# Optimization experiments

Measured on AMD Instinct MI355X. Metric: run time of the kernel, lower is better.

Reference implementation:

```python
import jax, jax.numpy as jnp
import numpy as np

B, T, IN, H, NB, OUT = 256, 2048, 128, 256, 4, 8
BS = H // NB  # branch size = 64


def setup_inputs() -> dict:
    key = jax.random.key(0)
    ks = jax.random.split(key, 7)
    x = jax.random.normal(ks[0], (B, T, IN), dtype=jnp.float32)
    Wb = jax.random.normal(ks[1], (NB, IN, BS), dtype=jnp.float32) * (1.0 / np.sqrt(IN))
    bb = jax.random.normal(ks[2], (NB, BS), dtype=jnp.float32) * 0.05
    Wo = jax.random.normal(ks[3], (H, OUT), dtype=jnp.float32) * (1.0 / np.sqrt(H))
    bo = jax.random.normal(ks[4], (OUT,), dtype=jnp.float32) * 0.05
    # tau_m ~ U(0,4); tau_n branch i ~ U(-4+2i, -1+2i) per the torch init
    tau_m = jax.random.uniform(ks[5], (H,), dtype=jnp.float32, minval=0.0, maxval=4.0)
    lo = (-4.0 + 2.0 * jnp.arange(NB, dtype=jnp.float32))[:, None]
    tau_n = lo + 3.0 * jax.random.uniform(ks[6], (NB, BS), dtype=jnp.float32)
    return {"x": x, "Wb": Wb, "bb": bb, "Wo": Wo, "bo": bo,
            "tau_m": tau_m, "tau_n": tau_n}


def reference(x, Wb, bb, Wo, bo, tau_m, tau_n):
    Bsz = x.shape[0]
    # Batch all per-step branch projections into one einsum: [B,T,NB,BS] -> [B,T,H]
    # (branch i writes slice [i*BS:(i+1)*BS], which matches the reshape order)
    D = jnp.einsum('bti,nis->btns', x, Wb) + bb  # [B,T,NB,BS]
    D = D.reshape(Bsz, x.shape[1], -1)           # [B,T,H]

    beta = jax.nn.sigmoid(tau_n).reshape(-1)     # [H], per-branch smoothing
    alpha = jax.nn.sigmoid(tau_m)                # [H]

    def step(carry, d_t):
        c, m = carry
        c = beta * c + (1.0 - beta) * d_t        # dendritic current EMA
        m = alpha * m + (1.0 - alpha) * c        # membrane EMA
        o = jax.nn.sigmoid(m @ Wo + bo)          # [B,OUT]
        return (c, m), o

    init = (jnp.zeros((Bsz, D.shape[-1]), D.dtype),
            jnp.zeros((Bsz, D.shape[-1]), D.dtype))
    _, outs = jax.lax.scan(step, init, jnp.swapaxes(D, 0, 1))  # outs: [T,B,OUT]
    return jnp.swapaxes(outs, 0, 1)              # [B,T,OUT]
```

## Files before the change

kernel.cpp:

```cpp
#include <hip/hip_runtime.h>
#include <hip/hip_bf16.h>
#include <math.h>

#define DEVFN __device__ __forceinline__

typedef __attribute__((ext_vector_type(8))) __bf16 bf16x8;
typedef __attribute__((ext_vector_type(8))) short s16x8;
typedef __attribute__((ext_vector_type(4))) float f32x4;
typedef __attribute__((ext_vector_type(4))) unsigned int u32x4;

constexpr int Tt    = 2048;
constexpr int INt   = 128;
constexpr int Ht    = 256;
constexpr int OUTt  = 8;
constexpr int TT    = 64;
constexpr int NTILE = 32;

union Frag {
  s16x8 s;
  bf16x8 b;
  u32x4 u;
};

DEVFN unsigned short f2bf(float f) {
  unsigned int u = __builtin_bit_cast(unsigned int, f);
  u += 0x7fffu + ((u >> 16) & 1u);
  return (unsigned short)(u >> 16);
}

DEVFN unsigned int pack2(float lo, float hi) {
  return (unsigned int)f2bf(lo) | ((unsigned int)f2bf(hi) << 16);
}

__global__
__attribute__((amdgpu_flat_work_group_size(1024, 1024)))
void sfnn_fused(
    const float* __restrict__ x, const float* __restrict__ Wb,
    const float* __restrict__ bb, const float* __restrict__ Wo,
    const float* __restrict__ bo, const float* __restrict__ tau_m,
    const float* __restrict__ tau_n, float* __restrict__ out)
{
  const int b    = blockIdx.x;
  const int tid  = threadIdx.x;
  const int lane = tid & 63;
  const int w    = tid >> 6;
  const int l16  = lane & 15;
  const int lhi  = lane >> 4;
  const int sid  = tid - 512;

  const int tg = w >> 3;
  const int hg = w & 7;

  __shared__ __align__(16) unsigned char  Xb[2][TT * 256];
  __shared__ __align__(16) float          DfT[Ht * TT];
  __shared__ __align__(16) unsigned short Mb[TT * Ht];
  __shared__ __align__(16) unsigned short WoT[16 * Ht];

  {
    const int j  = w;
    const int k0 = 4 * (tid & 63);
    float v0 = 0.f, v1 = 0.f, v2 = 0.f, v3 = 0.f;
    if (j < OUTt) {
      v0 = Wo[(k0 + 0) * OUTt + j]; v1 = Wo[(k0 + 1) * OUTt + j];
      v2 = Wo[(k0 + 2) * OUTt + j]; v3 = Wo[(k0 + 3) * OUTt + j];
    }
    unsigned long long pk = (unsigned long long)pack2(v0, v1) |
                            ((unsigned long long)pack2(v2, v3) << 32);
    *(unsigned long long*)(&WoT[j * 256 + (k0 ^ ((j & 7) << 3))]) = pk;
  }

  Frag Wf[2][4];
  #pragma unroll
  for (int nh = 0; nh < 2; ++nh) {
    const int h = 32 * hg + 16 * nh + l16;
    const int n = h >> 6, s = h & 63;
    #pragma unroll
    for (int ks = 0; ks < 4; ++ks) {
      #pragma unroll
      for (int j = 0; j < 8; ++j) {
        const int i = 32 * ks + 8 * lhi + j;
        Wf[nh][ks].s[j] = (short)f2bf(Wb[(n * 128 + i) * 64 + s]);
      }
    }
  }

  float beta = 0.f, alpha = 0.f, omb = 0.f, oma = 0.f, bbh = 0.f;
  if (tid < 256) {
    beta  = 1.f / (1.f + expf(-tau_n[tid]));
    alpha = 1.f / (1.f + expf(-tau_m[tid]));
    omb   = 1.f - beta;
    oma   = 1.f - alpha;
    bbh   = bb[tid];
  }
  float bo_l = 0.f;
  if (w >= 4 && w < 8) bo_l = (l16 < OUTt) ? bo[l16] : 0.f;

  const float* xb   = x   + (size_t)b * Tt * INt;
  float*       outb = out + (size_t)b * Tt * OUTt;

  float c_s = 0.f, m_s = 0.f;
  f32x4 dacc[2][2];
  f32x4 Q0, Q1;

  #define BAR() do {                                                       \
    asm volatile("s_waitcnt lgkmcnt(0)" ::: "memory");                     \
    __builtin_amdgcn_s_barrier();                                          \
  } while (0)

  #define WAITVM(N) do {                                                   \
    asm volatile("s_waitcnt vmcnt(" #N ")" ::: "memory");                  \
    __builtin_amdgcn_sched_barrier(0);                                     \
  } while (0)

  #define ISSUE(TILE) do {                                                 \
    const float* _p = xb + (size_t)(TILE) * (TT * INt) + 4 * (size_t)sid;  \
    asm volatile("global_load_dwordx4 %0, %1, off" : "=&v"(Q0) : "v"(_p));        \
    asm volatile("global_load_dwordx4 %0, %1, off" : "=&v"(Q1) : "v"(_p + 2048)); \
  } while (0)

  #define STAGE(BUF, TILE) do {                                            \
    const int kb = 8 * (sid & 31);                                         \
    WAITVM(0);                                                             \
    {                                                                      \
      const int t = (sid >> 5);                                            \
      unsigned long long pk = (unsigned long long)pack2(Q0.x, Q0.y) |      \
            ((unsigned long long)pack2(Q0.z, Q0.w) << 32);                 \
      *(unsigned long long*)(&Xb[BUF][t * 256 + (kb ^ ((t & 7) << 4))]) = pk; \
    }                                                                      \
    {                                                                      \
      const int t = 16 + (sid >> 5);                                       \
      unsigned long long pk = (unsigned long long)pack2(Q1.x, Q1.y) |      \
            ((unsigned long long)pack2(Q1.z, Q1.w) << 32);                 \
      *(unsigned long long*)(&Xb[BUF][t * 256 + (kb ^ ((t & 7) << 4))]) = pk; \
    }                                                                      \
    const float* _p2 = xb + (size_t)(TILE) * (TT * INt) + 4 * (size_t)sid; \
    asm volatile("global_load_dwordx4 %0, %1, off" : "=&v"(Q0) : "v"(_p2 + 4096)); \
    asm volatile("global_load_dwordx4 %0, %1, off" : "=&v"(Q1) : "v"(_p2 + 6144)); \
    WAITVM(0);                                                             \
    {                                                                      \
      const int t = 32 + (sid >> 5);                                       \
      unsigned long long pk = (unsigned long long)pack2(Q0.x, Q0.y) |      \
            ((unsigned long long)pack2(Q0.z, Q0.w) << 32);                 \
      *(unsigned long long*)(&Xb[BUF][t * 256 + (kb ^ ((t & 7) << 4))]) = pk; \
    }                                                                      \
    {                                                                      \
      const int t = 48 + (sid >> 5);                                       \
      unsigned long long pk = (unsigned long long)pack2(Q1.x, Q1.y) |      \
            ((unsigned long long)pack2(Q1.z, Q1.w) << 32);                 \
      *(unsigned long long*)(&Xb[BUF][t * 256 + (kb ^ ((t & 7) << 4))]) = pk; \
    }                                                                      \
  } while (0)

  #define GEMM(BUF) do {                                                   \
    _Pragma("unroll")                                                      \
    for (int tt = 0; tt < 2; ++tt) {                                       \
      _Pragma("unroll")                                                    \
      for (int nh = 0; nh < 2; ++nh) dacc[tt][nh] = f32x4{0.f,0.f,0.f,0.f};\
      const int row = 32 * tg + 16 * tt + l16;                             \
      const int rs = row * 256, sw = (row & 7) << 4;                       \
      _Pragma("unroll")                                                    \
      for (int ks = 0; ks < 4; ++ks) {                                     \
        Frag a;                                                            \
        a.u = *(const u32x4*)(&Xb[BUF][rs + ((64 * ks + 16 * lhi) ^ sw)]); \
        _Pragma("unroll")                                                  \
        for (int nh = 0; nh < 2; ++nh)                                     \
          dacc[tt][nh] = __builtin_amdgcn_mfma_f32_16x16x32_bf16(          \
              a.b, Wf[nh][ks].b, dacc[tt][nh], 0, 0, 0);                   \
      }                                                                    \
    }                                                                      \
  } while (0)

  #define WRITEDF() do {                                                   \
    _Pragma("unroll")                                                      \
    for (int tt = 0; tt < 2; ++tt)                                         \
      _Pragma("unroll")                                                    \
      for (int nh = 0; nh < 2; ++nh) {                                     \
        const int h = 32 * hg + 16 * nh + l16;                             \
        const int qi = 8 * tg + 4 * tt + lhi;                              \
        *(f32x4*)(&DfT[h * 64 + ((4 * qi) ^ ((h & 7) << 2))]) =            \
            dacc[tt][nh];                                                  \
      }                                                                    \
  } while (0)

  #define SCAN() do {                                                      \
    if (tid < 256) {                                                       \
      const int hb = tid * 64, dsw = (tid & 7) << 2;                       \
      _Pragma("unroll")                                                    \
      for (int gg = 0; gg < 4; ++gg) {                                     \
        f32x4 dv[4];                                                       \
        _Pragma("unroll")                                                  \
        for (int q = 0; q < 4; ++q)                                        \
          dv[q] = *(const f32x4*)(&DfT[hb + ((16 * gg + 4 * q) ^ dsw)]);   \
        _Pragma("unroll")                                                  \
        for (int q = 0; q < 4; ++q)                                        \
          _Pragma("unroll")                                                \
          for (int r = 0; r < 4; ++r) {                                    \
            const int t = 16 * gg + 4 * q + r;                             \
            const float d = dv[q][r] + bbh;                                \
            c_s = fmaf(beta, c_s, omb * d);                                \
            m_s = fmaf(alpha, m_s, oma * c_s);                             \
            Mb[t * 256 + (tid ^ ((t & 7) << 3))] = f2bf(m_s);              \
          }                                                                \
      }                                                                    \
    }                                                                      \
  } while (0)

  #define PROJ(TI) do {                                                    \
    const int tp = w - 4;                                                  \
    const int trow = 16 * tp + l16;                                        \
    const int mrb = trow * 256, msw = (trow & 7) << 3;                     \
    const int wrb = l16 * 256,  wsw = (l16 & 7) << 3;                      \
    f32x4 p = f32x4{0.f, 0.f, 0.f, 0.f};                                   \
    _Pragma("unroll")                                                      \
    for (int ks = 0; ks < 8; ++ks) {                                       \
      const int k0 = 32 * ks + 8 * lhi;                                    \
      Frag ma, wo;                                                         \
      ma.u = *(const u32x4*)(&Mb[mrb + (k0 ^ msw)]);                       \
      wo.u = *(const u32x4*)(&WoT[wrb + (k0 ^ wsw)]);                      \
      p = __builtin_amdgcn_mfma_f32_16x16x32_bf16(ma.b, wo.b, p, 0, 0, 0); \
    }                                                                      \
    if (l16 < OUTt) {                                                      \
      _Pragma("unroll")                                                    \
      for (int r = 0; r < 4; ++r) {                                        \
        const int t = 16 * tp + 4 * lhi + r;                               \
        outb[(size_t)((TI) * TT + t) * OUTt + l16] =                       \
            1.f / (1.f + __expf(-(p[r] + bo_l)));                          \
      }                                                                    \
    }                                                                      \
  } while (0)

  if (w >= 8) {
    ISSUE(0); STAGE(0, 0);
    ISSUE(1); STAGE(1, 1);
  }
  BAR();
  GEMM(0);

  #define ITER(I, DOPROJ, DOGEMM, DOIS) do {                               \
    if ((DOIS) && w >= 8) ISSUE((I) + 2);                                  \
    WRITEDF();                                                             \
    if ((DOPROJ) && w >= 4 && w < 8) PROJ((I) - 1);                        \
    if (DOGEMM) GEMM(((I) + 1) & 1);                                       \
    BAR();                                                         \
    SCAN();                                                                \
    if ((DOIS) && w >= 8) STAGE((I) & 1, (I) + 2);                         \
    BAR();                                                         \
  } while (0)

  ITER(0, 0, 1, 1);
  for (int I = 1; I <= 29; ++I) ITER(I, 1, 1, 1);
  ITER(30, 1, 1, 0);
  ITER(31, 1, 0, 0);
  if (w >= 4 && w < 8) PROJ(31);

  #undef ISSUE
  #undef STAGE
  #undef GEMM
  #undef WRITEDF
  #undef SCAN
  #undef PROJ
  #undef ITER
  #undef BAR
  #undef WAITVM
}

extern "C" void kernel_launch(void* const* d_in, const int* in_sizes, int n_in,
                              void* d_out, int out_size, void* d_ws, size_t ws_size,
                              hipStream_t stream) {
  const float* x     = (const float*)d_in[0];
  const float* Wb    = (const float*)d_in[1];
  const float* bb    = (const float*)d_in[2];
  const float* Wo    = (const float*)d_in[3];
  const float* bo    = (const float*)d_in[4];
  const float* tau_m = (const float*)d_in[5];
  const float* tau_n = (const float*)d_in[6];
  float* out = (float*)d_out;

  sfnn_fused<<<dim3(256), dim3(1024), 0, stream>>>(x, Wb, bb, Wo, bo, tau_m, tau_n, out);
}
```

Measured before the change: 102.0 us.

## Restructure into a three-stage software pipeline with smaller time tiles

```diff
diff --git a/kernel.cpp b/kernel.cpp
--- a/kernel.cpp
+++ b/kernel.cpp
@@ -13,8 +13,8 @@
 constexpr int INt   = 128;
 constexpr int Ht    = 256;
 constexpr int OUTt  = 8;
-constexpr int TT    = 64;
-constexpr int NTILE = 32;
+constexpr int TT    = 32;
+constexpr int NTILE = 64;
 
 union Frag {
   s16x8 s;
@@ -48,12 +48,9 @@
   const int lhi  = lane >> 4;
   const int sid  = tid - 512;
 
-  const int tg = w >> 3;
-  const int hg = w & 7;
-
-  __shared__ __align__(16) unsigned char  Xb[2][TT * 256];
-  __shared__ __align__(16) float          DfT[Ht * TT];
-  __shared__ __align__(16) unsigned short Mb[TT * Ht];
+  __shared__ __align__(16) unsigned char  Xb[3][TT * 256];
+  __shared__ __align__(16) float          DfT[2][Ht * TT];
+  __shared__ __align__(16) unsigned short Mb[2][TT * Ht];
   __shared__ __align__(16) unsigned short WoT[16 * Ht];
 
   {
@@ -69,17 +66,16 @@
     *(unsigned long long*)(&WoT[j * 256 + (k0 ^ ((j & 7) << 3))]) = pk;
   }
 
-  Frag Wf[2][4];
-  #pragma unroll
-  for (int nh = 0; nh < 2; ++nh) {
-    const int h = 32 * hg + 16 * nh + l16;
+  Frag Wf[4];
+  {
+    const int h = 16 * w + l16;
     const int n = h >> 6, s = h & 63;
     #pragma unroll
     for (int ks = 0; ks < 4; ++ks) {
       #pragma unroll
       for (int j = 0; j < 8; ++j) {
         const int i = 32 * ks + 8 * lhi + j;
-        Wf[nh][ks].s[j] = (short)f2bf(Wb[(n * 128 + i) * 64 + s]);
+        Wf[ks].s[j] = (short)f2bf(Wb[(n * 128 + i) * 64 + s]);
       }
     }
   }
@@ -93,14 +89,14 @@
     bbh   = bb[tid];
   }
   float bo_l = 0.f;
-  if (w >= 4 && w < 8) bo_l = (l16 < OUTt) ? bo[l16] : 0.f;
+  if (w == 4 || w == 5) bo_l = (l16 < OUTt) ? bo[l16] : 0.f;
 
   const float* xb   = x   + (size_t)b * Tt * INt;
   float*       outb = out + (size_t)b * Tt * OUTt;
 
   float c_s = 0.f, m_s = 0.f;
-  f32x4 dacc[2][2];
-  f32x4 Q0, Q1;
+  f32x4 dacc[2];
+  f32x4 QA0, QA1, QB0, QB1;
 
   #define BAR() do {                                                       \
     asm volatile("s_waitcnt lgkmcnt(0)" ::: "memory");                     \
@@ -112,15 +108,14 @@
     __builtin_amdgcn_sched_barrier(0);                                     \
   } while (0)
 
-  #define ISSUE(TILE) do {                                                 \
+  #define ISSUE(TILE, Q0, Q1) do {                                         \
     const float* _p = xb + (size_t)(TILE) * (TT * INt) + 4 * (size_t)sid;  \
     asm volatile("global_load_dwordx4 %0, %1, off" : "=&v"(Q0) : "v"(_p));        \
     asm volatile("global_load_dwordx4 %0, %1, off" : "=&v"(Q1) : "v"(_p + 2048)); \
   } while (0)
 
-  #define STAGE(BUF, TILE) do {                                            \
+  #define STAGEWR(BUF, Q0, Q1) do {                                        \
     const int kb = 8 * (sid & 31);                                         \
-    WAITVM(0);                                                             \
     {                                                                      \
       const int t = (sid >> 5);                                            \
       unsigned long long pk = (unsigned long long)pack2(Q0.x, Q0.y) |      \
@@ -133,79 +128,57 @@
             ((unsigned long long)pack2(Q1.z, Q1.w) << 32);                 \
       *(unsigned long long*)(&Xb[BUF][t * 256 + (kb ^ ((t & 7) << 4))]) = pk; \
     }                                                                      \
-    const float* _p2 = xb + (size_t)(TILE) * (TT * INt) + 4 * (size_t)sid; \
-    asm volatile("global_load_dwordx4 %0, %1, off" : "=&v"(Q0) : "v"(_p2 + 4096)); \
-    asm volatile("global_load_dwordx4 %0, %1, off" : "=&v"(Q1) : "v"(_p2 + 6144)); \
-    WAITVM(0);                                                             \
-    {                                                                      \
-      const int t = 32 + (sid >> 5);                                       \
-      unsigned long long pk = (unsigned long long)pack2(Q0.x, Q0.y) |      \
-            ((unsigned long long)pack2(Q0.z, Q0.w) << 32);                 \
-      *(unsigned long long*)(&Xb[BUF][t * 256 + (kb ^ ((t & 7) << 4))]) = pk; \
-    }                                                                      \
-    {                                                                      \
-      const int t = 48 + (sid >> 5);                                       \
-      unsigned long long pk = (unsigned long long)pack2(Q1.x, Q1.y) |      \
-            ((unsigned long long)pack2(Q1.z, Q1.w) << 32);                 \
-      *(unsigned long long*)(&Xb[BUF][t * 256 + (kb ^ ((t & 7) << 4))]) = pk; \
-    }                                                                      \
   } while (0)
 
   #define GEMM(BUF) do {                                                   \
     _Pragma("unroll")                                                      \
     for (int tt = 0; tt < 2; ++tt) {                                       \
-      _Pragma("unroll")                                                    \
-      for (int nh = 0; nh < 2; ++nh) dacc[tt][nh] = f32x4{0.f,0.f,0.f,0.f};\
-      const int row = 32 * tg + 16 * tt + l16;                             \
+      dacc[tt] = f32x4{0.f, 0.f, 0.f, 0.f};                                \
+      const int row = 16 * tt + l16;                                       \
       const int rs = row * 256, sw = (row & 7) << 4;                       \
       _Pragma("unroll")                                                    \
       for (int ks = 0; ks < 4; ++ks) {                                     \
         Frag a;                                                            \
         a.u = *(const u32x4*)(&Xb[BUF][rs + ((64 * ks + 16 * lhi) ^ sw)]); \
-        _Pragma("unroll")                                                  \
-        for (int nh = 0; nh < 2; ++nh)                                     \
-          dacc[tt][nh] = __builtin_amdgcn_mfma_f32_16x16x32_bf16(          \
-              a.b, Wf[nh][ks].b, dacc[tt][nh], 0, 0, 0);                   \
+        dacc[tt] = __builtin_amdgcn_mfma_f32_16x16x32_bf16(                \
+            a.b, Wf[ks].b, dacc[tt], 0, 0, 0);                             \
       }                                                                    \
     }                                                                      \
   } while (0)
 
-  #define WRITEDF() do {                                                   \
+  #define WRITEDF(BUF) do {                                                \
+    const int h = 16 * w + l16;                                            \
     _Pragma("unroll")                                                      \
-    for (int tt = 0; tt < 2; ++tt)                                         \
+    for (int tt = 0; tt < 2; ++tt) {                                       \
+      const int qi = 4 * tt + lhi;                                         \
+      *(f32x4*)(&DfT[BUF][h * 32 + ((qi ^ (h & 7)) << 2)]) = dacc[tt];     \
+    }                                                                      \
+  } while (0)
+
+  #define SCAN(BUF) do {                                                   \
+    if (tid < 256) {                                                       \
+      const int hb = tid * 32, h7 = tid & 7;                               \
       _Pragma("unroll")                                                    \
-      for (int nh = 0; nh < 2; ++nh) {                                     \
-        const int h = 32 * hg + 16 * nh + l16;                             \
-        const int qi = 8 * tg + 4 * tt + lhi;                              \
-        *(f32x4*)(&DfT[h * 64 + ((4 * qi) ^ ((h & 7) << 2))]) =            \
-            dacc[tt][nh];                                                  \
-      }                                                                    \
-  } while (0)
-
-  #define SCAN() do {                                                      \
-    if (tid < 256) {                                                       \
-      const int hb = tid * 64, dsw = (tid & 7) << 2;                       \
-      _Pragma("unroll")                                                    \
-      for (int gg = 0; gg < 4; ++gg) {                                     \
+      for (int g = 0; g < 2; ++g) {                                        \
         f32x4 dv[4];                                                       \
         _Pragma("unroll")                                                  \
         for (int q = 0; q < 4; ++q)                                        \
-          dv[q] = *(const f32x4*)(&DfT[hb + ((16 * gg + 4 * q) ^ dsw)]);   \
+          dv[q] = *(const f32x4*)(&DfT[BUF][hb + (((4 * g + q) ^ h7) << 2)]); \
         _Pragma("unroll")                                                  \
         for (int q = 0; q < 4; ++q)                                        \
           _Pragma("unroll")                                                \
           for (int r = 0; r < 4; ++r) {                                    \
-            const int t = 16 * gg + 4 * q + r;                             \
+            const int t = 16 * g + 4 * q + r;                              \
             const float d = dv[q][r] + bbh;                                \
             c_s = fmaf(beta, c_s, omb * d);                                \
             m_s = fmaf(alpha, m_s, oma * c_s);                             \
-            Mb[t * 256 + (tid ^ ((t & 7) << 3))] = f2bf(m_s);              \
+            Mb[BUF][t * 256 + (tid ^ ((t & 7) << 3))] = f2bf(m_s);         \
           }                                                                \
       }                                                                    \
     }                                                                      \
   } while (0)
 
-  #define PROJ(TI) do {                                                    \
+  #define PROJ(TI, BUF) do {                                               \
     const int tp = w - 4;                                                  \
     const int trow = 16 * tp + l16;                                        \
     const int mrb = trow * 256, msw = (trow & 7) << 3;                     \
@@ -215,7 +188,7 @@
     for (int ks = 0; ks < 8; ++ks) {                                       \
       const int k0 = 32 * ks + 8 * lhi;                                    \
       Frag ma, wo;                                                         \
-      ma.u = *(const u32x4*)(&Mb[mrb + (k0 ^ msw)]);                       \
+      ma.u = *(const u32x4*)(&Mb[BUF][mrb + (k0 ^ msw)]);                  \
       wo.u = *(const u32x4*)(&WoT[wrb + (k0 ^ wsw)]);                      \
       p = __builtin_amdgcn_mfma_f32_16x16x32_bf16(ma.b, wo.b, p, 0, 0, 0); \
     }                                                                      \
@@ -229,37 +202,51 @@
     }                                                                      \
   } while (0)
 
+  #define ITER_EV(I, DOG, DOS, DOP, DOISS, DOSTG, WN) do {                 \
+    if ((DOISS) && w >= 8) ISSUE((I) + 2, QA0, QA1);                       \
+    if (DOG) { GEMM((I) % 3); WRITEDF((I) & 1); }                          \
+    if ((DOS) && w < 4) SCAN(((I) - 1) & 1);                               \
+    if ((DOP) && (w == 4 || w == 5)) PROJ((I) - 2, (I) & 1);               \
+    if ((DOSTG) && w >= 8) { WAITVM(WN); STAGEWR(((I) + 1) % 3, QB0, QB1); } \
+    BAR();                                                                 \
+  } while (0)
+
+  #define ITER_OD(I, DOG, DOS, DOP, DOISS, DOSTG, WN) do {                 \
+    if ((DOISS) && w >= 8) ISSUE((I) + 2, QB0, QB1);                       \
+    if (DOG) { GEMM((I) % 3); WRITEDF((I) & 1); }                          \
+    if ((DOS) && w < 4) SCAN(((I) - 1) & 1);                               \
+    if ((DOP) && (w == 4 || w == 5)) PROJ((I) - 2, (I) & 1);               \
+    if ((DOSTG) && w >= 8) { WAITVM(WN); STAGEWR(((I) + 1) % 3, QA0, QA1); } \
+    BAR();                                                                 \
+  } while (0)
+
   if (w >= 8) {
-    ISSUE(0); STAGE(0, 0);
-    ISSUE(1); STAGE(1, 1);
+    ISSUE(0, QA0, QA1);
+    WAITVM(0);
+    STAGEWR(0, QA0, QA1);
+    ISSUE(1, QB0, QB1);
   }
   BAR();
-  GEMM(0);
-
-  #define ITER(I, DOPROJ, DOGEMM, DOIS) do {                               \
-    if ((DOIS) && w >= 8) ISSUE((I) + 2);                                  \
-    WRITEDF();                                                             \
-    if ((DOPROJ) && w >= 4 && w < 8) PROJ((I) - 1);                        \
-    if (DOGEMM) GEMM(((I) + 1) & 1);                                       \
-    BAR();                                                         \
-    SCAN();                                                                \
-    if ((DOIS) && w >= 8) STAGE((I) & 1, (I) + 2);                         \
-    BAR();                                                         \
-  } while (0)
-
-  ITER(0, 0, 1, 1);
-  for (int I = 1; I <= 29; ++I) ITER(I, 1, 1, 1);
-  ITER(30, 1, 1, 0);
-  ITER(31, 1, 0, 0);
-  if (w >= 4 && w < 8) PROJ(31);
+
+  ITER_EV(0, 1, 0, 0, 1, 1, 2);
+  ITER_OD(1, 1, 1, 0, 1, 1, 2);
+  for (int jj = 1; jj <= 30; ++jj) {
+    ITER_EV(2 * jj,     1, 1, 1, 1, 1, 2);
+    ITER_OD(2 * jj + 1, 1, 1, 1, 1, 1, 2);
+  }
+  ITER_EV(62, 1, 1, 1, 0, 1, 0);
+  ITER_OD(63, 1, 1, 1, 0, 0, 0);
+  ITER_EV(64, 0, 1, 1, 0, 0, 0);
+  ITER_OD(65, 0, 0, 1, 0, 0, 0);
 
   #undef ISSUE
-  #undef STAGE
+  #undef STAGEWR
   #undef GEMM
   #undef WRITEDF
   #undef SCAN
   #undef PROJ
-  #undef ITER
+  #undef ITER_EV
+  #undef ITER_OD
   #undef BAR
   #undef WAITVM
 }
```

New measurement: 96.59 us. 5.3% less time.
